# Optimization experiments

Hardware: AMD Instinct MI355X
Metric: run time of the kernel (lower is better)

## Reference

```python
import jax, jax.numpy as jnp
import numpy as np

B = 131072   # batch
K = 3        # kernel size (= stride)
NP = 9       # num patches (9x9 image, 3x3 kernel, stride 3)
NU = 81      # num logic units/kernels
NOPS = 16    # real-valued binary logic ops


def setup_inputs() -> dict:
    key = jax.random.key(0)
    k1, k2, k3, k4 = jax.random.split(key, 4)
    x = jax.random.uniform(k1, (B, 1, 9, 9), dtype=jnp.float32)          # soft-binary image
    sel_a_logits = jax.random.normal(k2, (NU, K * K), dtype=jnp.float32)  # input-A selector per unit
    sel_b_logits = jax.random.normal(k3, (NU, K * K), dtype=jnp.float32)  # input-B selector per unit
    op_logits = jax.random.normal(k4, (NU, NOPS), dtype=jnp.float32)      # logic-op mixture per unit
    return {"x": x, "sel_a_logits": sel_a_logits, "sel_b_logits": sel_b_logits, "op_logits": op_logits}


def _soft_logic_mix(a, b, w):
    # a, b: [B, NU] soft-binary operands; w: [NU, 16] op mixture weights (broadcast over batch).
    # The 16 real-valued binary logic gates (Petersen et al. differentiable logic networks).
    ab = a * b
    return (w[:, 1] * ab
            + w[:, 2] * (a - ab)
            + w[:, 3] * a
            + w[:, 4] * (b - ab)
            + w[:, 5] * b
            + w[:, 6] * (a + b - 2.0 * ab)      # xor
            + w[:, 7] * (a + b - ab)            # or
            + w[:, 8] * (1.0 - (a + b - ab))    # nor
            + w[:, 9] * (1.0 - (a + b - 2.0 * ab))  # xnor
            + w[:, 10] * (1.0 - b)
            + w[:, 11] * (1.0 - b + ab)
            + w[:, 12] * (1.0 - a)
            + w[:, 13] * (1.0 - a + ab)
            + w[:, 14] * (1.0 - ab)             # nand
            + w[:, 15])                          # op 0 contributes 0


def reference(x, sel_a_logits, sel_b_logits, op_logits):
    b_sz = x.shape[0]
    img = x[:, 0]  # [B, 9, 9]
    # unfold(2,K,S).unfold(3,K,S) with S == K == 3 -> non-overlapping 3x3 patches, row-major patch order
    patches = img.reshape(b_sz, NP // K, K, NP // K, K)
    patches = patches.transpose(0, 1, 3, 2, 4).reshape(b_sz, NP, K * K)  # [B, 9, 9]
    # unit u uses patch u // kernels_per_pos (kernels_per_pos = 81 // 9 = 9)
    unit2patch = jnp.arange(NU) // (NU // NP)
    inp = patches[:, unit2patch]  # [B, 81, 9]
    a = jnp.einsum('bui,ui->bu', inp, jax.nn.softmax(sel_a_logits, axis=-1))  # [B, 81]
    b = jnp.einsum('bui,ui->bu', inp, jax.nn.softmax(sel_b_logits, axis=-1))  # [B, 81]
    w = jax.nn.softmax(op_logits, axis=-1)  # [81, 16]
    return _soft_logic_mix(a, b, w)  # [B, 81]
```

## Files before the change

kernel.cpp:

```cpp
#include <hip/hip_runtime.h>
#include <math.h>


#define NB      131072
#define NUNITS  81
#define BPB     64
#define THREADS 256
#define NBLK    (NB / BPB)
#define REC     24
#define CHUNKS  1296

__global__ __launch_bounds__(256)
void logic_prep_kernel(const float* __restrict__ sa_logits,
                       const float* __restrict__ sb_logits,
                       const float* __restrict__ op_logits,
                       float* __restrict__ tab)
{
    const int tid = threadIdx.x;
    if (tid < 81) {
        const int u = tid;
        float v[9], m = -1e30f;
        #pragma unroll
        for (int i = 0; i < 9; ++i) { v[i] = sa_logits[u * 9 + i]; m = fmaxf(m, v[i]); }
        float s = 0.f;
        #pragma unroll
        for (int i = 0; i < 9; ++i) { v[i] = expf(v[i] - m); s += v[i]; }
        const float r = 1.f / s;
        #pragma unroll
        for (int i = 0; i < 9; ++i) tab[u * REC + i] = v[i] * r;
    } else if (tid < 162) {
        const int u = tid - 81;
        float v[9], m = -1e30f;
        #pragma unroll
        for (int i = 0; i < 9; ++i) { v[i] = sb_logits[u * 9 + i]; m = fmaxf(m, v[i]); }
        float s = 0.f;
        #pragma unroll
        for (int i = 0; i < 9; ++i) { v[i] = expf(v[i] - m); s += v[i]; }
        const float r = 1.f / s;
        #pragma unroll
        for (int i = 0; i < 9; ++i) tab[u * REC + 9 + i] = v[i] * r;
    } else if (tid < 243) {
        const int u = tid - 162;
        float v[16], m = -1e30f;
        #pragma unroll
        for (int i = 0; i < 16; ++i) { v[i] = op_logits[u * 16 + i]; m = fmaxf(m, v[i]); }
        float s = 0.f;
        #pragma unroll
        for (int i = 0; i < 16; ++i) { v[i] = expf(v[i] - m); s += v[i]; }
        const float r = 1.f / s;
        #pragma unroll
        for (int i = 0; i < 16; ++i) v[i] *= r;
        const float cab = v[1] - v[2] - v[4] - 2.f*v[6] - v[7] + v[8] + 2.f*v[9]
                        + v[11] + v[13] - v[14];
        const float ca  = v[2] + v[3] + v[6] + v[7] - v[8] - v[9] - v[12] - v[13];
        const float cb  = v[4] + v[5] + v[6] + v[7] - v[8] - v[9] - v[10] - v[11];
        const float c0  = v[8] + v[9] + v[10] + v[11] + v[12] + v[13] + v[14] + v[15];
        tab[u * REC + 18] = cab;
        tab[u * REC + 19] = ca;
        tab[u * REC + 20] = cb;
        tab[u * REC + 21] = c0;
    }
}

__global__ __launch_bounds__(THREADS)
void logic_main_kernel(const float* __restrict__ x,
                       const float* __restrict__ tab,
                       float* __restrict__ out)
{
    __shared__ float s_tile[BPB * 81];

    const int tid  = threadIdx.x;
    const int lane = tid & 63;
    const int wavei = __builtin_amdgcn_readfirstlane(tid >> 6);
    const size_t b0 = (size_t)blockIdx.x * BPB;

    {
        const float4* gsrc = (const float4*)(x + b0 * 81);
        float4* s4 = (float4*)s_tile;
        #pragma unroll
        for (int k = 0; k < 6; ++k) {
            int j = tid + k * THREADS;
            if (j < CHUNKS) s4[j] = gsrc[j];
        }
    }
    __syncthreads();

    if (wavei < 3) {
        float* my = s_tile + lane * 81 + wavei * 27;

        float in[27];
        #pragma unroll
        for (int j = 0; j < 27; ++j) in[j] = my[j];

        const float* __restrict__ wt = tab + wavei * 27 * REC;

        #pragma unroll
        for (int j = 0; j < 27; ++j) {
            const int q = j / 9;
            const float* __restrict__ wr = wt + j * REC;
            float a = 0.f, b = 0.f;
            #pragma unroll
            for (int i = 0; i < 9; ++i) {
                const float xi = in[q * 3 + (i / 3) * 9 + (i % 3)];
                a = fmaf(xi, wr[i],     a);
                b = fmaf(xi, wr[9 + i], b);
            }
            const float ab = a * b;
            my[j] = fmaf(wr[18], ab, fmaf(wr[19], a, fmaf(wr[20], b, wr[21])));
        }
    }

    __syncthreads();

    {
        const float4* s4 = (const float4*)s_tile;
        float4* gdst = (float4*)(out + b0 * 81);
        #pragma unroll
        for (int k = 0; k < 6; ++k) {
            int j = tid + k * THREADS;
            if (j < CHUNKS) gdst[j] = s4[j];
        }
    }
}

extern "C" void kernel_launch(void* const* d_in, const int* in_sizes, int n_in,
                              void* d_out, int out_size, void* d_ws, size_t ws_size,
                              hipStream_t stream)
{
    const float* x  = (const float*)d_in[0];
    const float* sa = (const float*)d_in[1];
    const float* sb = (const float*)d_in[2];
    const float* op = (const float*)d_in[3];
    float* tab = (float*)d_ws;
    float* outp = (float*)d_out;

    logic_prep_kernel<<<1, 256, 0, stream>>>(sa, sb, op, tab);
    logic_main_kernel<<<NBLK, THREADS, 0, stream>>>(x, tab, outp);
}
```

Baseline: 32.80 us.

## Process two tiles per block and prefetch the second during compute

```diff
diff --git a/kernel.cpp b/kernel.cpp
--- a/kernel.cpp
+++ b/kernel.cpp
@@ -6,7 +6,7 @@
 #define NUNITS  81
 #define BPB     64
 #define THREADS 256
-#define NBLK    (NB / BPB)
+#define NBLK    1024
 #define REC     24
 #define CHUNKS  1296
 
@@ -62,29 +62,10 @@
     }
 }
 
-__global__ __launch_bounds__(THREADS)
-void logic_main_kernel(const float* __restrict__ x,
-                       const float* __restrict__ tab,
-                       float* __restrict__ out)
+__device__ __forceinline__
+void compute_tile(float* __restrict__ s_tile, const float* __restrict__ tab,
+                  int lane, int wavei)
 {
-    __shared__ float s_tile[BPB * 81];
-
-    const int tid  = threadIdx.x;
-    const int lane = tid & 63;
-    const int wavei = __builtin_amdgcn_readfirstlane(tid >> 6);
-    const size_t b0 = (size_t)blockIdx.x * BPB;
-
-    {
-        const float4* gsrc = (const float4*)(x + b0 * 81);
-        float4* s4 = (float4*)s_tile;
-        #pragma unroll
-        for (int k = 0; k < 6; ++k) {
-            int j = tid + k * THREADS;
-            if (j < CHUNKS) s4[j] = gsrc[j];
-        }
-    }
-    __syncthreads();
-
     if (wavei < 3) {
         float* my = s_tile + lane * 81 + wavei * 27;
 
@@ -109,16 +90,80 @@
             my[j] = fmaf(wr[18], ab, fmaf(wr[19], a, fmaf(wr[20], b, wr[21])));
         }
     }
+}
 
+__global__ __launch_bounds__(THREADS)
+void logic_main_kernel(const float* __restrict__ x,
+                       const float* __restrict__ tab,
+                       float* __restrict__ out)
+{
+    __shared__ float s_tile[BPB * 81];
+
+    const int tid   = threadIdx.x;
+    const int lane  = tid & 63;
+    const int wavei = __builtin_amdgcn_readfirstlane(tid >> 6);
+    const int bid   = blockIdx.x;
+
+    const float4* __restrict__ x4   = (const float4*)x;
+    float4* __restrict__       out4 = (float4*)out;
+    float4* s4 = (float4*)s_tile;
+
+    float4 r[6];
+
+    {
+        const float4* g = x4 + (size_t)bid * CHUNKS;
+        #pragma unroll
+        for (int k = 0; k < 6; ++k) {
+            int j = tid + k * THREADS;
+            if (j < CHUNKS) r[k] = g[j];
+        }
+    }
+
+    #pragma unroll
+    for (int k = 0; k < 6; ++k) {
+        int j = tid + k * THREADS;
+        if (j < CHUNKS) s4[j] = r[k];
+    }
     __syncthreads();
 
     {
-        const float4* s4 = (const float4*)s_tile;
-        float4* gdst = (float4*)(out + b0 * 81);
+        const float4* g = x4 + (size_t)(bid + NBLK) * CHUNKS;
         #pragma unroll
         for (int k = 0; k < 6; ++k) {
             int j = tid + k * THREADS;
-            if (j < CHUNKS) gdst[j] = s4[j];
+            if (j < CHUNKS) r[k] = g[j];
+        }
+    }
+
+    compute_tile(s_tile, tab, lane, wavei);
+    __syncthreads();
+
+    {
+        float4* g = out4 + (size_t)bid * CHUNKS;
+        #pragma unroll
+        for (int k = 0; k < 6; ++k) {
+            int j = tid + k * THREADS;
+            if (j < CHUNKS) g[j] = s4[j];
+        }
+    }
+    __syncthreads();
+
+    #pragma unroll
+    for (int k = 0; k < 6; ++k) {
+        int j = tid + k * THREADS;
+        if (j < CHUNKS) s4[j] = r[k];
+    }
+    __syncthreads();
+
+    compute_tile(s_tile, tab, lane, wavei);
+    __syncthreads();
+
+    {
+        float4* g = out4 + (size_t)(bid + NBLK) * CHUNKS;
+        #pragma unroll
+        for (int k = 0; k < 6; ++k) {
+            int j = tid + k * THREADS;
+            if (j < CHUNKS) g[j] = s4[j];
         }
     }
 }
```

After: 42.78 us. 1.3x slower.

## Fuse softmax table prep into main kernel, computed per block by fourth wave

Applied to the files above, without the earlier changes.

```diff
diff --git a/kernel.cpp b/kernel.cpp
--- a/kernel.cpp
+++ b/kernel.cpp
@@ -10,79 +10,75 @@
 #define REC     24
 #define CHUNKS  1296
 
-__global__ __launch_bounds__(256)
-void logic_prep_kernel(const float* __restrict__ sa_logits,
-                       const float* __restrict__ sb_logits,
-                       const float* __restrict__ op_logits,
-                       float* __restrict__ tab)
-{
-    const int tid = threadIdx.x;
-    if (tid < 81) {
-        const int u = tid;
-        float v[9], m = -1e30f;
-        #pragma unroll
-        for (int i = 0; i < 9; ++i) { v[i] = sa_logits[u * 9 + i]; m = fmaxf(m, v[i]); }
-        float s = 0.f;
-        #pragma unroll
-        for (int i = 0; i < 9; ++i) { v[i] = expf(v[i] - m); s += v[i]; }
-        const float r = 1.f / s;
-        #pragma unroll
-        for (int i = 0; i < 9; ++i) tab[u * REC + i] = v[i] * r;
-    } else if (tid < 162) {
-        const int u = tid - 81;
-        float v[9], m = -1e30f;
-        #pragma unroll
-        for (int i = 0; i < 9; ++i) { v[i] = sb_logits[u * 9 + i]; m = fmaxf(m, v[i]); }
-        float s = 0.f;
-        #pragma unroll
-        for (int i = 0; i < 9; ++i) { v[i] = expf(v[i] - m); s += v[i]; }
-        const float r = 1.f / s;
-        #pragma unroll
-        for (int i = 0; i < 9; ++i) tab[u * REC + 9 + i] = v[i] * r;
-    } else if (tid < 243) {
-        const int u = tid - 162;
-        float v[16], m = -1e30f;
-        #pragma unroll
-        for (int i = 0; i < 16; ++i) { v[i] = op_logits[u * 16 + i]; m = fmaxf(m, v[i]); }
-        float s = 0.f;
-        #pragma unroll
-        for (int i = 0; i < 16; ++i) { v[i] = expf(v[i] - m); s += v[i]; }
-        const float r = 1.f / s;
-        #pragma unroll
-        for (int i = 0; i < 16; ++i) v[i] *= r;
-        const float cab = v[1] - v[2] - v[4] - 2.f*v[6] - v[7] + v[8] + 2.f*v[9]
-                        + v[11] + v[13] - v[14];
-        const float ca  = v[2] + v[3] + v[6] + v[7] - v[8] - v[9] - v[12] - v[13];
-        const float cb  = v[4] + v[5] + v[6] + v[7] - v[8] - v[9] - v[10] - v[11];
-        const float c0  = v[8] + v[9] + v[10] + v[11] + v[12] + v[13] + v[14] + v[15];
-        tab[u * REC + 18] = cab;
-        tab[u * REC + 19] = ca;
-        tab[u * REC + 20] = cb;
-        tab[u * REC + 21] = c0;
-    }
-}
-
 __global__ __launch_bounds__(THREADS)
-void logic_main_kernel(const float* __restrict__ x,
-                       const float* __restrict__ tab,
-                       float* __restrict__ out)
+void logic_fused_kernel(const float* __restrict__ x,
+                        const float* __restrict__ sa_logits,
+                        const float* __restrict__ sb_logits,
+                        const float* __restrict__ op_logits,
+                        float* __restrict__ out)
 {
     __shared__ float s_tile[BPB * 81];
+    __shared__ float s_tab[NUNITS * REC];
 
-    const int tid  = threadIdx.x;
-    const int lane = tid & 63;
+    const int tid   = threadIdx.x;
+    const int lane  = tid & 63;
     const int wavei = __builtin_amdgcn_readfirstlane(tid >> 6);
     const size_t b0 = (size_t)blockIdx.x * BPB;
 
-    {
+    if (wavei < 3) {
         const float4* gsrc = (const float4*)(x + b0 * 81);
         float4* s4 = (float4*)s_tile;
+        const int t3 = wavei * 64 + lane;
         #pragma unroll
-        for (int k = 0; k < 6; ++k) {
-            int j = tid + k * THREADS;
+        for (int k = 0; k < 7; ++k) {
+            int j = t3 + k * 192;
             if (j < CHUNKS) s4[j] = gsrc[j];
         }
+    } else {
+        for (int u = lane; u < NUNITS; u += 64) {
+            float v[9], m = -1e30f;
+            #pragma unroll
+            for (int i = 0; i < 9; ++i) { v[i] = sa_logits[u * 9 + i]; m = fmaxf(m, v[i]); }
+            float s = 0.f;
+            #pragma unroll
+            for (int i = 0; i < 9; ++i) { v[i] = expf(v[i] - m); s += v[i]; }
+            const float r = 1.f / s;
+            #pragma unroll
+            for (int i = 0; i < 9; ++i) s_tab[u * REC + i] = v[i] * r;
+        }
+        for (int u = lane; u < NUNITS; u += 64) {
+            float v[9], m = -1e30f;
+            #pragma unroll
+            for (int i = 0; i < 9; ++i) { v[i] = sb_logits[u * 9 + i]; m = fmaxf(m, v[i]); }
+            float s = 0.f;
+            #pragma unroll
+            for (int i = 0; i < 9; ++i) { v[i] = expf(v[i] - m); s += v[i]; }
+            const float r = 1.f / s;
+            #pragma unroll
+            for (int i = 0; i < 9; ++i) s_tab[u * REC + 9 + i] = v[i] * r;
+        }
+        for (int u = lane; u < NUNITS; u += 64) {
+            float v[16], m = -1e30f;
+            #pragma unroll
+            for (int i = 0; i < 16; ++i) { v[i] = op_logits[u * 16 + i]; m = fmaxf(m, v[i]); }
+            float s = 0.f;
+            #pragma unroll
+            for (int i = 0; i < 16; ++i) { v[i] = expf(v[i] - m); s += v[i]; }
+            const float r = 1.f / s;
+            #pragma unroll
+            for (int i = 0; i < 16; ++i) v[i] *= r;
+            const float cab = v[1] - v[2] - v[4] - 2.f*v[6] - v[7] + v[8] + 2.f*v[9]
+                            + v[11] + v[13] - v[14];
+            const float ca  = v[2] + v[3] + v[6] + v[7] - v[8] - v[9] - v[12] - v[13];
+            const float cb  = v[4] + v[5] + v[6] + v[7] - v[8] - v[9] - v[10] - v[11];
+            const float c0  = v[8] + v[9] + v[10] + v[11] + v[12] + v[13] + v[14] + v[15];
+            s_tab[u * REC + 18] = cab;
+            s_tab[u * REC + 19] = ca;
+            s_tab[u * REC + 20] = cb;
+            s_tab[u * REC + 21] = c0;
+        }
     }
+
     __syncthreads();
 
     if (wavei < 3) {
@@ -92,7 +88,7 @@
         #pragma unroll
         for (int j = 0; j < 27; ++j) in[j] = my[j];
 
-        const float* __restrict__ wt = tab + wavei * 27 * REC;
+        const float* __restrict__ wt = s_tab + wavei * 27 * REC;
 
         #pragma unroll
         for (int j = 0; j < 27; ++j) {
@@ -131,9 +127,7 @@
     const float* sa = (const float*)d_in[1];
     const float* sb = (const float*)d_in[2];
     const float* op = (const float*)d_in[3];
-    float* tab = (float*)d_ws;
     float* outp = (float*)d_out;
 
-    logic_prep_kernel<<<1, 256, 0, stream>>>(sa, sb, op, tab);
-    logic_main_kernel<<<NBLK, THREADS, 0, stream>>>(x, tab, outp);
+    logic_fused_kernel<<<NBLK, THREADS, 0, stream>>>(x, sa, sb, op, outp);
 }
```

Result: faster. 30.65 us (-6.5%).

## Load input tile directly to LDS and vectorize weight table reads

Applied to the files above, without the earlier changes.

```diff
diff --git a/kernel.cpp b/kernel.cpp
--- a/kernel.cpp
+++ b/kernel.cpp
@@ -8,7 +8,10 @@
 #define THREADS 256
 #define NBLK    (NB / BPB)
 #define REC     24
-#define CHUNKS  1296
+#define CHUNKS  (BPB * 81 / 4)
+
+typedef __attribute__((address_space(1))) const void GAS;
+typedef __attribute__((address_space(3))) void LAS;
 
 __global__ __launch_bounds__(256)
 void logic_prep_kernel(const float* __restrict__ sa_logits,
@@ -62,25 +65,28 @@
     }
 }
 
-__global__ __launch_bounds__(THREADS)
+__global__ __launch_bounds__(THREADS, 7)
 void logic_main_kernel(const float* __restrict__ x,
                        const float* __restrict__ tab,
                        float* __restrict__ out)
 {
     __shared__ float s_tile[BPB * 81];
 
-    const int tid  = threadIdx.x;
-    const int lane = tid & 63;
+    const int tid   = threadIdx.x;
+    const int lane  = tid & 63;
     const int wavei = __builtin_amdgcn_readfirstlane(tid >> 6);
     const size_t b0 = (size_t)blockIdx.x * BPB;
 
     {
         const float4* gsrc = (const float4*)(x + b0 * 81);
-        float4* s4 = (float4*)s_tile;
         #pragma unroll
         for (int k = 0; k < 6; ++k) {
-            int j = tid + k * THREADS;
-            if (j < CHUNKS) s4[j] = gsrc[j];
+            const int j = tid + k * THREADS;
+            if (j < CHUNKS) {
+                float* lbase = s_tile + (size_t)(k * THREADS + wavei * 64) * 4;
+                __builtin_amdgcn_global_load_lds((GAS*)(gsrc + j), (LAS*)lbase,
+                                                 16, 0, 0);
+            }
         }
     }
     __syncthreads();
@@ -92,21 +98,28 @@
         #pragma unroll
         for (int j = 0; j < 27; ++j) in[j] = my[j];
 
-        const float* __restrict__ wt = tab + wavei * 27 * REC;
+        const float4* __restrict__ wt4 =
+            (const float4*)(tab + (size_t)wavei * 27 * REC);
 
         #pragma unroll
         for (int j = 0; j < 27; ++j) {
             const int q = j / 9;
-            const float* __restrict__ wr = wt + j * REC;
+            const float4 q0 = wt4[j * 6 + 0];
+            const float4 q1 = wt4[j * 6 + 1];
+            const float4 q2 = wt4[j * 6 + 2];
+            const float4 q3 = wt4[j * 6 + 3];
+            const float4 q4 = wt4[j * 6 + 4];
+            const float4 q5 = wt4[j * 6 + 5];
+            const float wa[9] = { q0.x, q0.y, q0.z, q0.w, q1.x, q1.y, q1.z, q1.w, q2.x };
+            const float wb[9] = { q2.y, q2.z, q2.w, q3.x, q3.y, q3.z, q3.w, q4.x, q4.y };
             float a = 0.f, b = 0.f;
             #pragma unroll
             for (int i = 0; i < 9; ++i) {
                 const float xi = in[q * 3 + (i / 3) * 9 + (i % 3)];
-                a = fmaf(xi, wr[i],     a);
-                b = fmaf(xi, wr[9 + i], b);
+                a = fmaf(xi, wa[i], a);
+                b = fmaf(xi, wb[i], b);
             }
-            const float ab = a * b;
-            my[j] = fmaf(wr[18], ab, fmaf(wr[19], a, fmaf(wr[20], b, wr[21])));
+            my[j] = fmaf(q4.z, a * b, fmaf(q4.w, a, fmaf(q5.x, b, q5.y)));
         }
     }
 
@@ -117,7 +130,7 @@
         float4* gdst = (float4*)(out + b0 * 81);
         #pragma unroll
         for (int k = 0; k < 6; ++k) {
-            int j = tid + k * THREADS;
+            const int j = tid + k * THREADS;
             if (j < CHUNKS) gdst[j] = s4[j];
         }
     }
@@ -131,7 +144,7 @@
     const float* sa = (const float*)d_in[1];
     const float* sb = (const float*)d_in[2];
     const float* op = (const float*)d_in[3];
-    float* tab = (float*)d_ws;
+    float* tab  = (float*)d_ws;
     float* outp = (float*)d_out;
 
     logic_prep_kernel<<<1, 256, 0, stream>>>(sa, sb, op, tab);
```

Result: faster. 30.10 us (-8.2%).
